# Kernel optimization log

Hardware: AMD Instinct MI355X
Metric: run time of the kernel (lower is better)

Reference implementation:

```python
import jax, jax.numpy as jnp
import numpy as np

B, T = 32, 128
D, H, HD = 512, 8, 64
FF, E, N = 2048, 8, 3
NF = 16            # Fourier features
VOCAB, FEAT = 119, 200
SCALE = 10.0
EPS = 1e-5


def layernorm(x, g, b):
    m = jnp.mean(x, axis=-1, keepdims=True)
    v = jnp.mean((x - m) ** 2, axis=-1, keepdims=True)
    return (x - m) * jax.lax.rsqrt(v + EPS) * g + b


def setup_inputs() -> dict:
    key = jax.random.key(0)
    ks = jax.random.split(key, 32)
    f32 = jnp.float32
    inp = {
        "src": jax.random.randint(ks[0], (B, T), 0, VOCAB),
        "frac": jax.random.uniform(ks[1], (B, T), dtype=f32),
        "embed_table": jax.random.normal(ks[2], (VOCAB, FEAT), f32),
        "W_m2v": jax.random.normal(ks[3], (FEAT, D), f32) * 0.05,
        "b_m2v": jnp.zeros((D,), f32),
        "pb_W": jax.random.normal(ks[4], (1, NF), f32) * 0.1,
        "pb_b": jax.random.uniform(ks[5], (NF,), f32) * 2 * np.pi,
        "pb_a": jax.random.normal(ks[6], (NF,), f32),
        "Wk": jax.random.normal(ks[7], (N, D, D), f32) * 0.03,
        "bk": jnp.zeros((N, D), f32),
        "Wv": jax.random.normal(ks[8], (N, D, D), f32) * 0.03,
        "bv": jnp.zeros((N, D), f32),
        "Wo": jax.random.normal(ks[9], (N, D, D), f32) * 0.03,
        "bo": jnp.zeros((N, D), f32),
        "ln1_g": jnp.ones((N, D), f32),
        "ln1_b": jnp.zeros((N, D), f32),
        "ln2_g": jnp.ones((N, D), f32),
        "ln2_b": jnp.zeros((N, D), f32),
        "gate_W": jax.random.normal(ks[10], (N, D, E), f32) * 0.05,
        "gate_b": jnp.zeros((N, E), f32),
        "eW1": jax.random.normal(ks[11], (N, E, D, FF), f32) * 0.03,
        "eb1": jnp.zeros((N, E, FF), f32),
        "eW2": jax.random.normal(ks[12], (N, E, FF, D), f32) * 0.02,
        "eb2": jnp.zeros((N, E, D), f32),
    }
    return inp


def reference(src, frac, embed_table, W_m2v, b_m2v, pb_W, pb_b, pb_a,
              Wk, bk, Wv, bv, Wo, bo, ln1_g, ln1_b, ln2_g, ln2_b,
              gate_W, gate_b, eW1, eb1, eW2, eb2):
    # Embedder: mat2vec lookup + linear projection
    x = embed_table[src] @ W_m2v + b_m2v                      # [B,T,D]

    # Fourier positional bias: pb[b,i,j] = cos((frac_j - frac_i)*scale * W + b) @ a
    diffs = (frac[:, None, :] - frac[:, :, None]) * SCALE     # [B,T,T]
    rff = jnp.cos(diffs[..., None] * pb_W[0] + pb_b)          # [B,T,T,NF]
    pb = rff @ pb_a                                           # [B,T,T]

    for i in range(N):
        # --- Fourier-bias attention ---
        K = (x @ Wk[i] + bk[i]).reshape(B, T, H, HD).transpose(0, 2, 1, 3)  # [B,H,T,HD]
        V = (x @ Wv[i] + bv[i]).reshape(B, T, H, HD).transpose(0, 2, 1, 3)
        # scores[b,h,i,j,d] = K[b,h,j,d] + pb[b,i,j]; weighted = sum_j scores*V
        # factor: sum_j K*V (indep of i) + sum_j pb[b,i,j]*V[b,h,j,d]
        kv = jnp.sum(K * V, axis=2)                           # [B,H,HD]
        pbv = jnp.einsum('bij,bhjd->bhid', pb, V)             # [B,H,T,HD]
        wv = (pbv + kv[:, :, None, :]).transpose(0, 2, 1, 3).reshape(B, T, D)
        x = layernorm(x + wv @ Wo[i] + bo[i], ln1_g[i], ln1_b[i])

        # --- MoE FFN, top-2 gating (eval mode: no dropout/noise) ---
        probs = jax.nn.softmax(x @ gate_W[i] + gate_b[i], axis=-1)   # [B,T,E]
        top2_s, top2_e = jax.lax.top_k(probs, 2)                     # [B,T,2]
        w = jnp.sum(jax.nn.one_hot(top2_e, E, dtype=x.dtype) * top2_s[..., None], axis=2)  # [B,T,E]
        h = jax.nn.relu(jnp.einsum('btd,edf->btef', x, eW1[i]) + eb1[i])  # [B,T,E,FF]
        eo = jnp.einsum('btef,efd->bted', h, eW2[i]) + eb2[i]             # [B,T,E,D]
        ff = jnp.einsum('bte,bted->btd', w, eo)
        x = layernorm(x + ff, ln2_g[i], ln2_b[i])
    return x
```

## Files before the change

### kernel.cpp

```cpp
#include <hip/hip_runtime.h>
#include <math.h>

#define B_    32
#define T_    128
#define D_    512
#define FF_   2048
#define E_    8
#define NL_   3
#define NF_   16
#define FEAT_ 200
#define BT_   4096

#define GB_   64
#define TPB_  (BT_ / GB_)

typedef short bf16x8 __attribute__((ext_vector_type(8)));
typedef float f32x4  __attribute__((ext_vector_type(4)));

__device__ inline unsigned short f2bf(float f) {
    unsigned u = __float_as_uint(f);
    unsigned r = (u + 0x7fffu + ((u >> 16) & 1u)) >> 16;
    return (unsigned short)r;
}
__device__ inline void split_bf(float f, unsigned short& h, unsigned short& l) {
    h = f2bf(f);
    float fh = __uint_as_float(((unsigned)h) << 16);
    l = f2bf(f - fh);
}

__device__ __forceinline__ void ld_g2l(const unsigned short* g, unsigned short* l)
{
    __builtin_amdgcn_global_load_lds(
        (const __attribute__((address_space(1))) unsigned int*)(uintptr_t)g,
        (__attribute__((address_space(3))) unsigned int*)(uintptr_t)l,
        16, 0, 0);
}

template <int MODE, bool SPLITOUT, bool RELU>
__global__ __launch_bounds__(512)
void mgemm_k(const unsigned short* __restrict__ Ah, const unsigned short* __restrict__ Al,
             const unsigned short* __restrict__ Bh, const unsigned short* __restrict__ Bl,
             const float* __restrict__ bias,
             float* __restrict__ Cf, unsigned short* __restrict__ Ch,
             unsigned short* __restrict__ Cl,
             int M, int K, int N, long strB, int strBias,
             const int* __restrict__ counts, const int* __restrict__ offsets,
             const int* __restrict__ tok_list)
{
    const int z  = blockIdx.z;
    const int m0 = blockIdx.y * 128, n0 = blockIdx.x * 128;
    int rows, rowoff = 0;
    if constexpr (MODE != 0) {
        rows = counts[z];
        if (m0 >= rows) return;
        rowoff = offsets[z];
    } else {
        rows = M;
    }
    const unsigned short* Bhb = Bh + (long)z * strB;
    const unsigned short* Blb = Bl + (long)z * strB;
    const float* biasb = bias + (long)z * strBias;

    __shared__ unsigned short S[2][4 * 4096];

    const int tid  = threadIdx.x;
    const int w    = tid >> 6, lane = tid & 63;
    const int wm = w & 3, wn = w >> 2;
    const int l15 = lane & 15, quad = lane >> 4;

    const int srow = tid >> 2;
    const int sseg = (tid & 3) ^ ((tid >> 3) & 3);
    const int lbW  = w * 512;

    long gaA;
    if constexpr (MODE == 1) {
        int m_a = m0 + srow; if (m_a >= rows) m_a = rows - 1;
        gaA = tok_list[z * BT_ + m_a];
    } else if constexpr (MODE == 2) {
        int m_a = m0 + srow; if (m_a >= rows) m_a = rows - 1;
        gaA = (long)rowoff + m_a;
    } else {
        gaA = m0 + srow;
    }
    const long aoff = gaA * (long)K + sseg * 8;
    const long boff = (long)(n0 + srow) * K + sseg * 8;

    f32x4 acc[2][4];
#pragma unroll
    for (int i = 0; i < 2; ++i)
#pragma unroll
        for (int j = 0; j < 4; ++j) acc[i][j] = (f32x4)0.f;

    const int xq = quad ^ ((l15 >> 1) & 3);

    {
        unsigned short* Sb = S[0];
        ld_g2l(Ah  + aoff, Sb + 0 * 4096 + lbW);
        ld_g2l(Al  + aoff, Sb + 1 * 4096 + lbW);
        ld_g2l(Bhb + boff, Sb + 2 * 4096 + lbW);
        ld_g2l(Blb + boff, Sb + 3 * 4096 + lbW);
    }

    unsigned short* Scur = S[0];
    unsigned short* Snxt = S[1];

    for (int k0 = 0; k0 < K; k0 += 32) {
        __syncthreads();

        if (k0 + 32 < K) {
            int kn = k0 + 32;
            ld_g2l(Ah  + aoff + kn, Snxt + 0 * 4096 + lbW);
            ld_g2l(Al  + aoff + kn, Snxt + 1 * 4096 + lbW);
            ld_g2l(Bhb + boff + kn, Snxt + 2 * 4096 + lbW);
            ld_g2l(Blb + boff + kn, Snxt + 3 * 4096 + lbW);
        }

        bf16x8 ah2[2], al2[2], bh4[4], bl4[4];
#pragma unroll
        for (int i = 0; i < 2; ++i) {
            int ro = (wm * 32 + i * 16 + l15) * 32 + xq * 8;
            ah2[i] = *(const bf16x8*)&Scur[0 * 4096 + ro];
            al2[i] = *(const bf16x8*)&Scur[1 * 4096 + ro];
        }
#pragma unroll
        for (int j = 0; j < 4; ++j) {
            int ro = (wn * 64 + j * 16 + l15) * 32 + xq * 8;
            bh4[j] = *(const bf16x8*)&Scur[2 * 4096 + ro];
            bl4[j] = *(const bf16x8*)&Scur[3 * 4096 + ro];
        }
#pragma unroll
        for (int i = 0; i < 2; ++i)
#pragma unroll
            for (int j = 0; j < 4; ++j) {
                acc[i][j] = __builtin_amdgcn_mfma_f32_16x16x32_bf16(al2[i], bh4[j], acc[i][j], 0, 0, 0);
                acc[i][j] = __builtin_amdgcn_mfma_f32_16x16x32_bf16(ah2[i], bl4[j], acc[i][j], 0, 0, 0);
                acc[i][j] = __builtin_amdgcn_mfma_f32_16x16x32_bf16(ah2[i], bh4[j], acc[i][j], 0, 0, 0);
            }

        unsigned short* t = Scur; Scur = Snxt; Snxt = t;
    }

#pragma unroll
    for (int i = 0; i < 2; ++i) {
#pragma unroll
        for (int r = 0; r < 4; ++r) {
            int gm = m0 + wm * 32 + i * 16 + quad * 4 + r;
            if (MODE != 0 && gm >= rows) continue;
            long crow = (MODE != 0) ? ((long)rowoff + gm) : (long)gm;
#pragma unroll
            for (int j = 0; j < 4; ++j) {
                int col = n0 + wn * 64 + j * 16 + l15;
                float v = acc[i][j][r] + biasb[col];
                if constexpr (RELU) v = fmaxf(v, 0.f);
                if constexpr (SPLITOUT) {
                    unsigned short h, l;
                    split_bf(v, h, l);
                    Ch[crow * (long)N + col] = h;
                    Cl[crow * (long)N + col] = l;
                } else {
                    Cf[crow * (long)N + col] = v;
                }
            }
        }
    }
}

template <bool WF32, bool SPLIT>
__global__ __launch_bounds__(256)
void gemm_k(const float* __restrict__ A, const float* __restrict__ Bm,
            const float* __restrict__ bias, float* __restrict__ C,
            unsigned short* __restrict__ Oh, unsigned short* __restrict__ Ol,
            int K, int lda, int ldb, int ldc,
            long strA, long strB, long strC, int strBias)
{
    const int z  = blockIdx.z;
    const int m0 = blockIdx.y * 64, n0 = blockIdx.x * 64;
    const float* Ab    = A    + (long)z * strA;
    const float* Bb    = Bm   + (long)z * strB;
    const float* biasb = bias + (long)z * strBias;

    __shared__ float As[16][68];
    __shared__ float Bs[16][64];

    const int tid = threadIdx.x;
    const int tx  = tid & 15, ty = tid >> 4;
    const int ar  = tid >> 2;
    const int akc = (tid & 3) * 4;
    const float* Arow = Ab + (long)(m0 + ar) * lda;
    const int bkr = tid >> 4;
    const int bnc = (tid & 15) * 4;

    float acc[4][4];
#pragma unroll
    for (int i = 0; i < 4; ++i)
#pragma unroll
        for (int j = 0; j < 4; ++j) acc[i][j] = 0.f;

    for (int k0 = 0; k0 < K; k0 += 16) {
        if (k0 + 16 <= K) {
            float4 a = *(const float4*)(Arow + k0 + akc);
            As[akc + 0][ar] = a.x; As[akc + 1][ar] = a.y;
            As[akc + 2][ar] = a.z; As[akc + 3][ar] = a.w;
        } else {
#pragma unroll
            for (int j = 0; j < 4; ++j) {
                int kk = k0 + akc + j;
                As[akc + j][ar] = (kk < K) ? Arow[kk] : 0.f;
            }
        }
        {
            int kk = k0 + bkr;
            float4 b;
            if (kk < K) b = *(const float4*)(Bb + (long)kk * ldb + n0 + bnc);
            else        b = make_float4(0.f, 0.f, 0.f, 0.f);
            *(float4*)&Bs[bkr][bnc] = b;
        }
        __syncthreads();
#pragma unroll
        for (int k = 0; k < 16; ++k) {
            float4 av = *(const float4*)&As[k][ty * 4];
            float4 bv = *(const float4*)&Bs[k][tx * 4];
            float am[4] = {av.x, av.y, av.z, av.w};
            float bn[4] = {bv.x, bv.y, bv.z, bv.w};
#pragma unroll
            for (int i = 0; i < 4; ++i)
#pragma unroll
                for (int j = 0; j < 4; ++j)
                    acc[i][j] = fmaf(am[i], bn[j], acc[i][j]);
        }
        __syncthreads();
    }
#pragma unroll
    for (int i = 0; i < 4; ++i) {
        long base = ((long)z * strC) + (long)(m0 + ty * 4 + i) * ldc + n0 + tx * 4;
        const float* bp = biasb + n0 + tx * 4;
#pragma unroll
        for (int j = 0; j < 4; ++j) {
            float v = acc[i][j] + bp[j];
            if constexpr (WF32) C[base + j] = v;
            if constexpr (SPLIT) {
                unsigned short h, l;
                split_bf(v, h, l);
                Oh[base + j] = h;
                Ol[base + j] = l;
            }
        }
    }
}

__global__ __launch_bounds__(256)
void transpose_split_k(const float* __restrict__ in,
                       unsigned short* __restrict__ oh, unsigned short* __restrict__ ol,
                       int R, int C, long strIn, long strOut)
{
    __shared__ float tile[32][33];
    const float* I = in + (long)blockIdx.z * strIn;
    unsigned short* OH = oh + (long)blockIdx.z * strOut;
    unsigned short* OL = ol + (long)blockIdx.z * strOut;
    int c0 = blockIdx.x * 32, r0 = blockIdx.y * 32;
    int tx = threadIdx.x & 31, ty = threadIdx.x >> 5;
#pragma unroll
    for (int i = 0; i < 4; ++i)
        tile[ty + i * 8][tx] = I[(long)(r0 + ty + i * 8) * C + c0 + tx];
    __syncthreads();
#pragma unroll
    for (int i = 0; i < 4; ++i) {
        unsigned short h, l;
        split_bf(tile[tx][ty + i * 8], h, l);
        long o = (long)(c0 + ty + i * 8) * R + r0 + tx;
        OH[o] = h; OL[o] = l;
    }
}

__global__ void bias_cat_k(const float* __restrict__ a, const float* __restrict__ b,
                           float* __restrict__ o)
{
    int i = blockIdx.x * 256 + threadIdx.x;
    o[i] = (i < D_) ? a[i] : b[i - D_];
}

__global__ void embed_gather_k(const int* __restrict__ src,
                               const float* __restrict__ table,
                               float* __restrict__ emb)
{
    int t = blockIdx.x;
    int v = src[t];
    for (int k = threadIdx.x; k < FEAT_; k += 256)
        emb[t * FEAT_ + k] = table[v * FEAT_ + k];
}

__global__ __launch_bounds__(256)
void pb_k(const float* __restrict__ frac, const float* __restrict__ pbW,
          const float* __restrict__ pbb, const float* __restrict__ pba,
          float* __restrict__ pb)
{
    int idx = blockIdx.x * 256 + threadIdx.x;
    int b = idx >> 14;
    int i = (idx >> 7) & 127;
    int j = idx & 127;
    float diff = (frac[b * T_ + j] - frac[b * T_ + i]) * 10.0f;
    float s = 0.f;
#pragma unroll
    for (int f = 0; f < NF_; ++f)
        s = fmaf(cosf(fmaf(diff, pbW[f], pbb[f])), pba[f], s);
    pb[idx] = s;
}

__global__ __launch_bounds__(256)
void kv_k(const float* __restrict__ KV, float* __restrict__ kv)
{
    int idx = blockIdx.x * 256 + threadIdx.x;
    int b = idx >> 9, c = idx & 511;
    const float* Kp = KV + (long)b * T_ * 1024 + c;
    float s = 0.f;
    for (int t = 0; t < T_; ++t) {
        const float* p = Kp + t * 1024;
        s = fmaf(p[0], p[D_], s);
    }
    kv[idx] = s;
}

__global__ __launch_bounds__(256)
void ln_res_k(const float* __restrict__ x, const float* __restrict__ add,
              const float* __restrict__ g, const float* __restrict__ b,
              float* __restrict__ out, unsigned short* __restrict__ oh,
              unsigned short* __restrict__ ol)
{
    int wave = threadIdx.x >> 6, lane = threadIdx.x & 63;
    int row = blockIdx.x * 4 + wave;
    const float* xr = x   + (long)row * D_ + lane * 8;
    const float* ar = add + (long)row * D_ + lane * 8;
    float v[8]; float s = 0.f;
#pragma unroll
    for (int j = 0; j < 8; ++j) { v[j] = xr[j] + ar[j]; s += v[j]; }
#pragma unroll
    for (int off = 32; off > 0; off >>= 1) s += __shfl_xor(s, off, 64);
    float mean = s * (1.f / D_);
    float q = 0.f;
#pragma unroll
    for (int j = 0; j < 8; ++j) { float d = v[j] - mean; q += d * d; }
#pragma unroll
    for (int off = 32; off > 0; off >>= 1) q += __shfl_xor(q, off, 64);
    float inv = rsqrtf(q * (1.f / D_) + 1e-5f);
    float* orow = out + (long)row * D_ + lane * 8;
    unsigned short* hrow = oh + (long)row * D_ + lane * 8;
    unsigned short* lrow = ol + (long)row * D_ + lane * 8;
#pragma unroll
    for (int j = 0; j < 8; ++j) {
        int c = lane * 8 + j;
        float o = (v[j] - mean) * inv * g[c] + b[c];
        orow[j] = o;
        unsigned short hh, ll;
        split_bf(o, hh, ll);
        hrow[j] = hh; lrow[j] = ll;
    }
}

__global__ __launch_bounds__(256)
void ln_moe_k(const float* __restrict__ x, const float* __restrict__ eo,
              const int* __restrict__ tok_slot, const float* __restrict__ tok_w,
              const int* __restrict__ offsets,
              const float* __restrict__ g, const float* __restrict__ b,
              float* __restrict__ out, unsigned short* __restrict__ oh,
              unsigned short* __restrict__ ol)
{
    int wave = threadIdx.x >> 6, lane = threadIdx.x & 63;
    int row = blockIdx.x * 4 + wave;
    int  c0 = tok_slot[row * 2], c1 = tok_slot[row * 2 + 1];
    float w0 = tok_w[row * 2],  w1 = tok_w[row * 2 + 1];
    long r0 = offsets[c0 >> 12] + (c0 & 4095);
    long r1 = offsets[c1 >> 12] + (c1 & 4095);
    const float* xr = x  + (long)row * D_ + lane * 8;
    const float* e0 = eo + r0 * D_ + lane * 8;
    const float* e1 = eo + r1 * D_ + lane * 8;
    float v[8]; float s = 0.f;
#pragma unroll
    for (int j = 0; j < 8; ++j) {
        v[j] = xr[j] + w0 * e0[j] + w1 * e1[j];
        s += v[j];
    }
#pragma unroll
    for (int off = 32; off > 0; off >>= 1) s += __shfl_xor(s, off, 64);
    float mean = s * (1.f / D_);
    float q = 0.f;
#pragma unroll
    for (int j = 0; j < 8; ++j) { float d = v[j] - mean; q += d * d; }
#pragma unroll
    for (int off = 32; off > 0; off >>= 1) q += __shfl_xor(q, off, 64);
    float inv = rsqrtf(q * (1.f / D_) + 1e-5f);
    float* orow = out + (long)row * D_ + lane * 8;
    unsigned short* hrow = oh + (long)row * D_ + lane * 8;
    unsigned short* lrow = ol + (long)row * D_ + lane * 8;
#pragma unroll
    for (int j = 0; j < 8; ++j) {
        int c = lane * 8 + j;
        float o = (v[j] - mean) * inv * g[c] + b[c];
        orow[j] = o;
        unsigned short hh, ll;
        split_bf(o, hh, ll);
        hrow[j] = hh; lrow[j] = ll;
    }
}

__global__ __launch_bounds__(256)
void gate_k(const float* __restrict__ x, const float* __restrict__ gW,
            const float* __restrict__ gb, int* __restrict__ counts,
            int* __restrict__ tok_list, int* __restrict__ tok_slot,
            float* __restrict__ tok_w)
{
    __shared__ int scnt[E_];
    __shared__ int sbase[E_];
    __shared__ int sent[TPB_][2];

    const int wave = threadIdx.x >> 6, lane = threadIdx.x & 63;
    const int e  = lane & 7;
    const int ch = lane >> 3;
    const int t0 = blockIdx.x * TPB_;

    if (threadIdx.x < E_) scnt[threadIdx.x] = 0;
    __syncthreads();

    for (int it = 0; it < TPB_ / 4; ++it) {
        const int tl = it * 4 + wave;
        const int t  = t0 + tl;

        const float4* x4 = (const float4*)(x + (long)t * D_ + ch * 64);
        const float*  wr = gW + (long)ch * 64 * E_ + e;
        float acc = 0.f;
#pragma unroll
        for (int d4 = 0; d4 < 16; ++d4) {
            float4 xv = x4[d4];
            acc = fmaf(xv.x, wr[(d4 * 4 + 0) * 8], acc);
            acc = fmaf(xv.y, wr[(d4 * 4 + 1) * 8], acc);
            acc = fmaf(xv.z, wr[(d4 * 4 + 2) * 8], acc);
            acc = fmaf(xv.w, wr[(d4 * 4 + 3) * 8], acc);
        }
        acc += __shfl_xor(acc, 8, 64);
        acc += __shfl_xor(acc, 16, 64);
        acc += __shfl_xor(acc, 32, 64);
        acc += gb[e];

        float lg[8];
#pragma unroll
        for (int ee = 0; ee < 8; ++ee)
            lg[ee] = __shfl(acc, (lane & 56) | ee, 64);

        float m = lg[0];
#pragma unroll
        for (int ee = 1; ee < 8; ++ee) m = fmaxf(m, lg[ee]);
        float p[8]; float s = 0.f;
#pragma unroll
        for (int ee = 0; ee < 8; ++ee) { p[ee] = expf(lg[ee] - m); s += p[ee]; }
        float inv = 1.f / s;
        int e1 = 0;
#pragma unroll
        for (int ee = 1; ee < 8; ++ee) if (p[ee] > p[e1]) e1 = ee;
        int e2 = (e1 == 0) ? 1 : 0;
#pragma unroll
        for (int ee = 0; ee < 8; ++ee) {
            if (ee == e1) continue;
            if (p[ee] > p[e2]) e2 = ee;
        }

        if (lane == 0) {
            int ls1 = atomicAdd(&scnt[e1], 1);
            int ls2 = atomicAdd(&scnt[e2], 1);
            sent[tl][0] = (e1 << 12) | ls1;
            sent[tl][1] = (e2 << 12) | ls2;
            tok_w[t * 2]     = p[e1] * inv;
            tok_w[t * 2 + 1] = p[e2] * inv;
        }
    }
    __syncthreads();

    if (threadIdx.x < E_)
        sbase[threadIdx.x] = atomicAdd(&counts[threadIdx.x], scnt[threadIdx.x]);
    __syncthreads();

    for (int tl = threadIdx.x; tl < TPB_; tl += 256) {
        const int t = t0 + tl;
#pragma unroll
        for (int kk = 0; kk < 2; ++kk) {
            int v    = sent[tl][kk];
            int ee   = v >> 12;
            int slot = sbase[ee] + (v & 4095);
            tok_list[ee * BT_ + slot] = t;
            tok_slot[t * 2 + kk] = (ee << 12) | slot;
        }
    }
}

__global__ void zero_counts_k(int* __restrict__ counts)
{
    if (threadIdx.x < E_) counts[threadIdx.x] = 0;
}

__global__ void scan_k(const int* __restrict__ counts, int* __restrict__ offsets)
{
    if (threadIdx.x == 0) {
        int s = 0;
        for (int e = 0; e < E_; ++e) { offsets[e] = s; s += counts[e]; }
    }
}

extern "C" void kernel_launch(void* const* d_in, const int* in_sizes, int n_in,
                              void* d_out, int out_size, void* d_ws, size_t ws_size,
                              hipStream_t stream)
{
    const int*   src   = (const int*)  d_in[0];
    const float* frac  = (const float*)d_in[1];
    const float* table = (const float*)d_in[2];
    const float* W_m2v = (const float*)d_in[3];
    const float* b_m2v = (const float*)d_in[4];
    const float* pbW   = (const float*)d_in[5];
    const float* pbb   = (const float*)d_in[6];
    const float* pba   = (const float*)d_in[7];
    const float* Wk    = (const float*)d_in[8];
    const float* bk    = (const float*)d_in[9];
    const float* Wv    = (const float*)d_in[10];
    const float* bv    = (const float*)d_in[11];
    const float* Wo    = (const float*)d_in[12];
    const float* bo    = (const float*)d_in[13];
    const float* ln1g  = (const float*)d_in[14];
    const float* ln1b  = (const float*)d_in[15];
    const float* ln2g  = (const float*)d_in[16];
    const float* ln2b  = (const float*)d_in[17];
    const float* gW    = (const float*)d_in[18];
    const float* gb    = (const float*)d_in[19];
    const float* eW1   = (const float*)d_in[20];
    const float* eb1   = (const float*)d_in[21];
    const float* eW2   = (const float*)d_in[22];
    const float* eb2   = (const float*)d_in[23];

    float* ws   = (float*)d_ws;
    float* x    = ws;  ws += (long)BT_ * D_;
    float* pb   = ws;  ws += (long)B_ * T_ * T_;
    float* eo   = ws;  ws += (long)2 * BT_ * D_;
    float* kv   = ws;  ws += B_ * D_;
    float* tokw = ws;  ws += 2 * BT_;
    float* kvbias = ws; ws += 2 * D_;
    unsigned short* us = (unsigned short*)ws;
    unsigned short* x_h   = us;  us += (long)BT_ * D_;
    unsigned short* x_l   = us;  us += (long)BT_ * D_;
    unsigned short* Wkv_h = us;  us += (long)2 * D_ * D_;
    unsigned short* Wkv_l = us;  us += (long)2 * D_ * D_;
    unsigned short* Wo_h  = us;  us += (long)D_ * D_;
    unsigned short* Wo_l  = us;  us += (long)D_ * D_;
    unsigned short* e1_h  = us;  us += (long)E_ * FF_ * D_;
    unsigned short* e1_l  = us;  us += (long)E_ * FF_ * D_;
    unsigned short* e2_h  = us;  us += (long)E_ * D_ * FF_;
    unsigned short* e2_l  = us;  us += (long)E_ * D_ * FF_;
    int* counts  = (int*)us;
    int* offsets = counts + 8;
    int* toklist = offsets + 8;
    int* tokslot = toklist + E_ * BT_;
    char* ar = (char*)(tokslot + 2 * BT_);
    ar = (char*)(((size_t)ar + 255) & ~(size_t)255);
    unsigned short* h_h = (unsigned short*)ar;
    unsigned short* h_l = h_h + (long)2 * BT_ * FF_;
    float* emb  = (float*)ar;
    float* KVb  = emb + (long)BT_ * FEAT_;
    float* tmp  = KVb + (long)BT_ * 2 * D_;
    unsigned short* wv_h = (unsigned short*)(tmp + (long)BT_ * D_);
    unsigned short* wv_l = wv_h + (long)BT_ * D_;

    embed_gather_k<<<BT_, 256, 0, stream>>>(src, table, emb);
    gemm_k<true, true><<<dim3(8, 64, 1), 256, 0, stream>>>(
        emb, W_m2v, b_m2v, x, x_h, x_l, FEAT_, FEAT_, D_, D_, 0, 0, 0, 0);

    pb_k<<<(B_ * T_ * T_) / 256, 256, 0, stream>>>(frac, pbW, pbb, pba, pb);

    for (int i = 0; i < NL_; ++i) {
        transpose_split_k<<<dim3(16, 16, 1), 256, 0, stream>>>(
            Wk + (long)i * D_ * D_, Wkv_h, Wkv_l, D_, D_, 0, 0);
        transpose_split_k<<<dim3(16, 16, 1), 256, 0, stream>>>(
            Wv + (long)i * D_ * D_, Wkv_h + (long)D_ * D_, Wkv_l + (long)D_ * D_,
            D_, D_, 0, 0);
        transpose_split_k<<<dim3(16, 16, 1), 256, 0, stream>>>(
            Wo + (long)i * D_ * D_, Wo_h, Wo_l, D_, D_, 0, 0);
        transpose_split_k<<<dim3(64, 16, E_), 256, 0, stream>>>(
            eW1 + (long)i * E_ * D_ * FF_, e1_h, e1_l, D_, FF_,
            (long)D_ * FF_, (long)FF_ * D_);
        transpose_split_k<<<dim3(16, 64, E_), 256, 0, stream>>>(
            eW2 + (long)i * E_ * FF_ * D_, e2_h, e2_l, FF_, D_,
            (long)FF_ * D_, (long)D_ * FF_);
        bias_cat_k<<<4, 256, 0, stream>>>(bk + i * D_, bv + i * D_, kvbias);

        mgemm_k<0, false, false><<<dim3(8, 32, 1), 512, 0, stream>>>(
            x_h, x_l, Wkv_h, Wkv_l, kvbias,
            KVb, nullptr, nullptr, BT_, D_, 2 * D_, 0, 0,
            nullptr, nullptr, nullptr);

        kv_k<<<(B_ * D_) / 256, 256, 0, stream>>>(KVb, kv);

        gemm_k<false, true><<<dim3(8, 2, B_), 256, 0, stream>>>(
            pb, KVb + D_, kv, nullptr, wv_h, wv_l, T_, T_, 2 * D_, D_,
            (long)T_ * T_, (long)T_ * 2 * D_, (long)T_ * D_, D_);

        mgemm_k<0, false, false><<<dim3(4, 32, 1), 512, 0, stream>>>(
            wv_h, wv_l, Wo_h, Wo_l, bo + i * D_,
            tmp, nullptr, nullptr, BT_, D_, D_, 0, 0, nullptr, nullptr, nullptr);

        ln_res_k<<<BT_ / 4, 256, 0, stream>>>(x, tmp, ln1g + i * D_, ln1b + i * D_,
                                              x, x_h, x_l);

        zero_counts_k<<<1, 64, 0, stream>>>(counts);
        gate_k<<<GB_, 256, 0, stream>>>(x, gW + (long)i * D_ * E_, gb + i * E_,
                                        counts, toklist, tokslot, tokw);
        scan_k<<<1, 1, 0, stream>>>(counts, offsets);

        mgemm_k<1, true, true><<<dim3(16, 32, E_), 512, 0, stream>>>(
            x_h, x_l, e1_h, e1_l, eb1 + (long)i * E_ * FF_,
            nullptr, h_h, h_l, 0, D_, FF_,
            (long)FF_ * D_, FF_, counts, offsets, toklist);
        mgemm_k<2, false, false><<<dim3(4, 32, E_), 512, 0, stream>>>(
            h_h, h_l, e2_h, e2_l, eb2 + (long)i * E_ * D_,
            eo, nullptr, nullptr, 0, FF_, D_,
            (long)D_ * FF_, D_, counts, offsets, toklist);

        float* dst = (i == NL_ - 1) ? (float*)d_out : x;
        ln_moe_k<<<BT_ / 4, 256, 0, stream>>>(x, eo, tokslot, tokw, offsets,
                                              ln2g + i * D_, ln2b + i * D_,
                                              dst, x_h, x_l);
    }
}
```

Before: 1.183 ms.

## Triple-buffer GEMM shared-memory tiles with explicit vmcnt waits

Moves the split-bf16 GEMM main loop from double to triple buffering in LDS. It prefetches two K-tiles ahead and replaces __syncthreads with an explicit s_waitcnt vmcnt plus s_barrier, so one tile's global loads can stay in flight while the next is computed. The cost is 50% more LDS per block (192KB to... 96KB total), which may cut occupancy. It also relies on hand-counted vmcnt values matching the loads issued per STAGE.

```diff
diff --git a/kernel.cpp b/kernel.cpp
--- a/kernel.cpp
+++ b/kernel.cpp
@@ -61,7 +61,7 @@
     const unsigned short* Blb = Bl + (long)z * strB;
     const float* biasb = bias + (long)z * strBias;
 
-    __shared__ unsigned short S[2][4 * 4096];
+    __shared__ unsigned short S[3][4 * 4096];
 
     const int tid  = threadIdx.x;
     const int w    = tid >> 6, lane = tid & 63;
@@ -93,28 +93,29 @@
 
     const int xq = quad ^ ((l15 >> 1) & 3);
 
-    {
-        unsigned short* Sb = S[0];
-        ld_g2l(Ah  + aoff, Sb + 0 * 4096 + lbW);
-        ld_g2l(Al  + aoff, Sb + 1 * 4096 + lbW);
-        ld_g2l(Bhb + boff, Sb + 2 * 4096 + lbW);
-        ld_g2l(Blb + boff, Sb + 3 * 4096 + lbW);
-    }
-
-    unsigned short* Scur = S[0];
-    unsigned short* Snxt = S[1];
-
+    auto STAGE = [&](int buf, int kk) {
+        unsigned short* Sb = S[buf];
+        ld_g2l(Ah  + aoff + kk, Sb + 0 * 4096 + lbW);
+        ld_g2l(Al  + aoff + kk, Sb + 1 * 4096 + lbW);
+        ld_g2l(Bhb + boff + kk, Sb + 2 * 4096 + lbW);
+        ld_g2l(Blb + boff + kk, Sb + 3 * 4096 + lbW);
+    };
+
+    STAGE(0, 0);
+    STAGE(1, 32);
+
+    int sb = 0;
     for (int k0 = 0; k0 < K; k0 += 32) {
-        __syncthreads();
-
-        if (k0 + 32 < K) {
-            int kn = k0 + 32;
-            ld_g2l(Ah  + aoff + kn, Snxt + 0 * 4096 + lbW);
-            ld_g2l(Al  + aoff + kn, Snxt + 1 * 4096 + lbW);
-            ld_g2l(Bhb + boff + kn, Snxt + 2 * 4096 + lbW);
-            ld_g2l(Blb + boff + kn, Snxt + 3 * 4096 + lbW);
-        }
-
+        if (k0 + 32 < K) asm volatile("s_waitcnt vmcnt(4)" ::: "memory");
+        else             asm volatile("s_waitcnt vmcnt(0)" ::: "memory");
+        asm volatile("s_barrier" ::: "memory");
+
+        if (k0 + 64 < K) {
+            int nb = sb + 2; if (nb >= 3) nb -= 3;
+            STAGE(nb, k0 + 64);
+        }
+
+        const unsigned short* Scur = S[sb];
         bf16x8 ah2[2], al2[2], bh4[4], bl4[4];
 #pragma unroll
         for (int i = 0; i < 2; ++i) {
@@ -137,7 +138,7 @@
                 acc[i][j] = __builtin_amdgcn_mfma_f32_16x16x32_bf16(ah2[i], bh4[j], acc[i][j], 0, 0, 0);
             }
 
-        unsigned short* t = Scur; Scur = Snxt; Snxt = t;
+        ++sb; if (sb >= 3) sb = 0;
     }
 
 #pragma unroll
```

Measured after the change: 1.238 ms. +4.7%, slower.
